# Performance work log

Measured on AMD Instinct MI355X. Metric: run time of the kernel, lower is better.

## Reference

```python
import jax, jax.numpy as jnp
import numpy as np

GRID_SIZE = 16
SPLINE_ORDER = 4
GRID_LO, GRID_HI = -1.0, 1.0
NUM_GRID = 2 * SPLINE_ORDER + GRID_SIZE + 1  # 25 knots
NUM_COEFFS = GRID_SIZE + SPLINE_ORDER        # 20 basis functions
B, IN_F, OUT_F = 2048, 512, 512


def _make_grid():
    h = (GRID_HI - GRID_LO) / GRID_SIZE
    t1 = -SPLINE_ORDER * h + GRID_LO
    t2 = (GRID_SIZE + SPLINE_ORDER + 1) * h + GRID_LO
    return jnp.linspace(t1, t2, NUM_GRID)


def _bspline_basis(x, grid):
    # x: [..., in]; returns [..., in, NUM_COEFFS] via De Boor recursion
    xe = x[..., None]
    bases = ((xe >= grid[:-1]) & (xe < grid[1:])).astype(x.dtype)
    for k in range(1, SPLINE_ORDER + 1):
        left = (xe - grid[:-k - 1]) / (grid[k:-1] - grid[:-k - 1]) * bases[..., :-1]
        right = (grid[k + 1:] - xe) / (grid[k + 1:] - grid[1:-k]) * bases[..., 1:]
        bases = left + right
    return bases


def setup_inputs() -> dict:
    key = jax.random.key(0)
    ks = jax.random.split(key, 5)
    fan = np.sqrt(1.0 / IN_F)
    return {
        "x": jax.random.normal(ks[0], (B, IN_F), jnp.float32),
        "prelu_weight": jax.random.normal(ks[1], (OUT_F, IN_F), jnp.float32) * 0.25,
        "base_weight": jax.random.uniform(ks[2], (OUT_F, IN_F), jnp.float32, -fan, fan),
        "spline_weight": jax.random.uniform(ks[3], (OUT_F, IN_F), jnp.float32, -fan, fan),
        "spline_coeffs": jax.random.normal(ks[4], (OUT_F, IN_F, NUM_COEFFS), jnp.float32) * 0.1,
    }


def reference(x, prelu_weight, base_weight, spline_weight, spline_coeffs):
    grid = _make_grid()
    xc = jnp.clip(x, GRID_LO, GRID_HI)
    pos = jax.nn.relu(xc)
    neg = xc - pos
    # base path: sum_j base_w[i,j]*(prelu_w[i,j]*neg[b,j] + pos[b,j])
    # fused: never materialize the [out, B, in] prelu output
    base = neg @ (base_weight * prelu_weight).T + pos @ base_weight.T  # [B, out]
    basis = _bspline_basis(xc, grid)  # [B, in, K]
    # spline path: fold spline_weight into coeffs, single contraction over (j,k)
    eff_coeffs = spline_weight[:, :, None] * spline_coeffs  # [out, in, K]
    spline = jnp.einsum('bjk,ijk->bi', basis, eff_coeffs)   # [B, out]
    return base + spline
```

## Files before the change

kernel.cpp:

```cpp
#include <hip/hip_runtime.h>


typedef _Float16 half_t;
typedef __attribute__((ext_vector_type(8))) _Float16 half8;
typedef __attribute__((ext_vector_type(4))) float floatx4;

#define B_DIM   2048
#define J_DIM   512
#define O_DIM   512
#define SLOTS   22
#define K_TOT   (J_DIM * SLOTS)
#define BM      256
#define BN      256
#define BK      32
#define KSPLIT  16

__device__ __forceinline__ void bspline5(float xc, int& k0, float Nv[5]) {
    const float invS = 7.68f;
    float u = (xc + 1.5f) * invS;
    int m = (int)u;
    m = min(max(m, 3), 19);
    k0 = m - 4;
    Nv[0] = 1.f; Nv[1] = 0.f; Nv[2] = 0.f; Nv[3] = 0.f; Nv[4] = 0.f;
#pragma unroll
    for (int d = 1; d <= 4; ++d) {
        float nw[5];
        float inv_d = 1.0f / (float)d;
#pragma unroll
        for (int r = 0; r < 5; ++r) {
            if (r > d) { nw[r] = 0.f; continue; }
            float kk = (float)(m - d + r);
            float acc = 0.f;
            if (r >= 1) acc += (u - kk) * Nv[r - 1];
            if (r < d)  acc += (kk + (float)(d + 1) - u) * Nv[r];
            nw[r] = acc * inv_d;
        }
#pragma unroll
        for (int r = 0; r < 5; ++r) Nv[r] = nw[r];
    }
}

__device__ __forceinline__ unsigned packh2(float a, float b) {
    half_t ha = (half_t)a, hb = (half_t)b;
    unsigned short ua = __builtin_bit_cast(unsigned short, ha);
    unsigned short ub = __builtin_bit_cast(unsigned short, hb);
    return (unsigned)ua | ((unsigned)ub << 16);
}

__global__ __launch_bounds__(256) void prep2(const float* __restrict__ x,
                                             const float* __restrict__ pw,
                                             const float* __restrict__ bw,
                                             const float* __restrict__ sw,
                                             const float* __restrict__ sc,
                                             half_t* __restrict__ A,
                                             half_t* __restrict__ Ct) {
    __shared__ half_t sbuf[2][128 * 88];
    int bid = blockIdx.x;
    int t = threadIdx.x;
    int sub = t >> 7;
    int jq  = t & 127;
    int j0  = jq * 4;

    if (bid < 256) {
        int i = bid * 2 + sub;
        size_t ij0 = (size_t)i * J_DIM + j0;
        float4 s4 = *(const float4*)(sw + ij0);
        float4 b4 = *(const float4*)(bw + ij0);
        float4 p4 = *(const float4*)(pw + ij0);
        const float4* sp4 = (const float4*)(sc + ij0 * 20);
        unsigned u[44];
#pragma unroll
        for (int jj = 0; jj < 4; ++jj) {
            float s = ((const float*)&s4)[jj];
            float b = ((const float*)&b4)[jj];
            float p = ((const float*)&p4)[jj];
#pragma unroll
            for (int v = 0; v < 5; ++v) {
                float4 c4 = sp4[jj * 5 + v];
                u[jj * 11 + v * 2 + 0] = packh2(s * c4.x, s * c4.y);
                u[jj * 11 + v * 2 + 1] = packh2(s * c4.z, s * c4.w);
            }
            u[jj * 11 + 10] = packh2(b * p, b);
        }
        uint4* dst = (uint4*)(Ct + (size_t)i * K_TOT + (size_t)j0 * SLOTS);
#pragma unroll
        for (int v = 0; v < 11; ++v)
            dst[v] = make_uint4(u[4 * v], u[4 * v + 1], u[4 * v + 2], u[4 * v + 3]);
        return;
    }

    int b0 = (bid - 256) * 2;
    int b = b0 + sub;
    float4 x4 = *(const float4*)(x + (size_t)b * J_DIM + j0);
    half_t* reg = &sbuf[sub][jq * 88];

    half8 z;
#pragma unroll
    for (int e = 0; e < 8; ++e) z[e] = (half_t)0.f;
#pragma unroll
    for (int v = 0; v < 11; ++v) *(half8*)(reg + v * 8) = z;

#pragma unroll
    for (int jj = 0; jj < 4; ++jj) {
        float xv = ((const float*)&x4)[jj];
        float xc = fminf(fmaxf(xv, -1.f), 1.f);
        float pos = fmaxf(xc, 0.f);
        float neg = xc - pos;
        int k0; float Nv[5];
        bspline5(xc, k0, Nv);
        half_t* rb = reg + jj * SLOTS;
#pragma unroll
        for (int rr = 0; rr < 5; ++rr) {
            int k = k0 + rr;
            if (k >= 0) rb[k] = (half_t)Nv[rr];
        }
        *(unsigned*)(rb + 20) = packh2(neg, pos);
    }
    __syncthreads();

    const uint4* src = (const uint4*)&sbuf[0][0];
    uint4* dst = (uint4*)(A + (size_t)b0 * K_TOT);
#pragma unroll
    for (int v = 0; v < 11; ++v) dst[v * 256 + t] = src[v * 256 + t];
}

__global__ __launch_bounds__(512, 2) void gemm256_f16(const half_t* __restrict__ A,
                                                      const half_t* __restrict__ Bt,
                                                      float* __restrict__ out) {
    constexpr int KS_LEN = K_TOT / KSPLIT;
    constexpr int KCH = KS_LEN / BK;

    __shared__ half_t As[3][BM * BK];
    __shared__ half_t Bs[3][BN * BK];

    int lid = blockIdx.x + 8 * (blockIdx.y + 2 * blockIdx.z);
    int c8 = lid & 7;
    int r2 = lid >> 3;
    int bz = c8 + 8 * (r2 & 1);
    int rr2 = r2 >> 1;
    int bx = rr2 & 7;
    int by = rr2 >> 3;

    int m0 = bx * BM;
    int n0 = by * BN;
    int ks = bz * KS_LEN;

    int t = threadIdx.x;
    int w = t >> 6;
    int l = t & 63;
    int wm = w >> 2, wn = w & 3;

    floatx4 acc[8][4] = {};

    int lrow = l >> 2;
    int lkof = (((l & 3) ^ ((l >> 3) & 3)) * 8);

    const half_t* gA = A + (size_t)m0 * K_TOT + ks;
    const half_t* gB = Bt + (size_t)n0 * K_TOT + ks;

    int q = l >> 4;
    int fr = l & 15;
    int qs = (q ^ ((fr >> 1) & 3)) * 8;

#define ISSUE_LOADS(c, p)                                                     \
    {                                                                         \
        int kb = (c) * BK;                                                    \
        _Pragma("unroll")                                                     \
        for (int s = 0; s < 2; ++s) {                                         \
            int r = (w * 2 + s) * 16 + lrow;                                  \
            __builtin_amdgcn_global_load_lds(                                 \
                (const __attribute__((address_space(1))) unsigned int*)       \
                    (gA + (size_t)r * K_TOT + kb + lkof),                     \
                (__attribute__((address_space(3))) unsigned int*)             \
                    (&As[p][0] + (w * 2 + s) * 512),                          \
                16, 0, 0);                                                    \
            __builtin_amdgcn_global_load_lds(                                 \
                (const __attribute__((address_space(1))) unsigned int*)       \
                    (gB + (size_t)r * K_TOT + kb + lkof),                     \
                (__attribute__((address_space(3))) unsigned int*)             \
                    (&Bs[p][0] + (w * 2 + s) * 512),                          \
                16, 0, 0);                                                    \
        }                                                                     \
    }

    ISSUE_LOADS(0, 0)
    ISSUE_LOADS(1, 1)

    int pb = 0;
    for (int c = 0; c < KCH; ++c) {
        if (c + 2 < KCH) {
            asm volatile("s_waitcnt vmcnt(4)" ::: "memory");
            __builtin_amdgcn_s_barrier();
            int pn = pb + 2; if (pn >= 3) pn -= 3;
            ISSUE_LOADS(c + 2, pn)
        } else if (c + 2 == KCH) {
            asm volatile("s_waitcnt vmcnt(4)" ::: "memory");
            __builtin_amdgcn_s_barrier();
        } else {
            asm volatile("s_waitcnt vmcnt(0)" ::: "memory");
            __builtin_amdgcn_s_barrier();
        }

        half8 af[8], bf[4];
#pragma unroll
        for (int nt = 0; nt < 4; ++nt)
            bf[nt] = *(const half8*)(&Bs[pb][0] + (wn * 64 + nt * 16 + fr) * BK + qs);
#pragma unroll
        for (int mt = 0; mt < 8; ++mt)
            af[mt] = *(const half8*)(&As[pb][0] + (wm * 128 + mt * 16 + fr) * BK + qs);

        __builtin_amdgcn_s_setprio(1);
#pragma unroll
        for (int mt = 0; mt < 8; ++mt)
#pragma unroll
            for (int nt = 0; nt < 4; ++nt)
                acc[mt][nt] = __builtin_amdgcn_mfma_f32_16x16x32_f16(
                    af[mt], bf[nt], acc[mt][nt], 0, 0, 0);
        __builtin_amdgcn_s_setprio(0);

        if (++pb == 3) pb = 0;
    }
#undef ISSUE_LOADS

    float* dst = out + (size_t)bz * ((size_t)B_DIM * O_DIM);
#pragma unroll
    for (int mt = 0; mt < 8; ++mt)
#pragma unroll
        for (int nt = 0; nt < 4; ++nt) {
            int rw = m0 + wm * 128 + mt * 16 + q * 4;
            int cc = n0 + wn * 64 + nt * 16 + fr;
#pragma unroll
            for (int rg = 0; rg < 4; ++rg)
                dst[(size_t)(rw + rg) * O_DIM + cc] = acc[mt][nt][rg];
        }
}

__global__ __launch_bounds__(256) void reduce16(const float* __restrict__ parts,
                                                float* __restrict__ out) {
    constexpr int N4 = B_DIM * O_DIM / 4;
    int i = blockIdx.x * 256 + threadIdx.x;
    const float4* p = (const float4*)parts;
    float4 a = p[i];
#pragma unroll
    for (int z = 1; z < KSPLIT; ++z) {
        float4 b = p[(size_t)z * N4 + i];
        a.x += b.x; a.y += b.y; a.z += b.z; a.w += b.w;
    }
    ((float4*)out)[i] = a;
}

__global__ __launch_bounds__(256) void kan_fallback(const float* __restrict__ x,
                                                    const float* __restrict__ pw,
                                                    const float* __restrict__ bw,
                                                    const float* __restrict__ sw,
                                                    const float* __restrict__ sc,
                                                    float* __restrict__ out) {
    __shared__ float s_neg[J_DIM], s_pos[J_DIM], s_bas[J_DIM][5];
    __shared__ int s_k0[J_DIM];
    int b = blockIdx.x;
    int t = threadIdx.x;
#pragma unroll
    for (int jj = 0; jj < 2; ++jj) {
        int j = t + jj * 256;
        float xv = x[(size_t)b * J_DIM + j];
        float xc = fminf(fmaxf(xv, -1.f), 1.f);
        float pos = fmaxf(xc, 0.f);
        s_pos[j] = pos;
        s_neg[j] = xc - pos;
        int k0; float Nv[5];
        bspline5(xc, k0, Nv);
        s_k0[j] = k0;
#pragma unroll
        for (int r = 0; r < 5; ++r) s_bas[j][r] = Nv[r];
    }
    __syncthreads();
    for (int i = t; i < O_DIM; i += 256) {
        float acc = 0.f;
        for (int j = 0; j < J_DIM; ++j) {
            size_t ij = (size_t)i * J_DIM + j;
            float bwv = bw[ij];
            acc += bwv * (pw[ij] * s_neg[j] + s_pos[j]);
            int k0 = s_k0[j];
            const float* cp = sc + ij * 20;
            float sp = 0.f;
#pragma unroll
            for (int r = 0; r < 5; ++r) {
                int k = k0 + r;
                if (k >= 0) sp += s_bas[j][r] * cp[k];
            }
            acc += sw[ij] * sp;
        }
        out[(size_t)b * O_DIM + i] = acc;
    }
}

extern "C" void kernel_launch(void* const* d_in, const int* in_sizes, int n_in,
                              void* d_out, int out_size, void* d_ws, size_t ws_size,
                              hipStream_t stream) {
    const float* x  = (const float*)d_in[0];
    const float* pw = (const float*)d_in[1];
    const float* bw = (const float*)d_in[2];
    const float* sw = (const float*)d_in[3];
    const float* sc = (const float*)d_in[4];
    float* out = (float*)d_out;

    const size_t abct = (size_t)(B_DIM + O_DIM) * K_TOT * sizeof(half_t);
    const size_t parts_bytes = (size_t)KSPLIT * B_DIM * O_DIM * sizeof(float);

    if (ws_size >= abct + parts_bytes) {
        half_t* A  = (half_t*)d_ws;
        half_t* Ct = A + (size_t)B_DIM * K_TOT;
        float* parts = (float*)((char*)d_ws + abct);

        prep2<<<256 + B_DIM / 2, 256, 0, stream>>>(x, pw, bw, sw, sc, A, Ct);
        dim3 g(B_DIM / BM, O_DIM / BN, KSPLIT);
        gemm256_f16<<<g, 512, 0, stream>>>(A, Ct, parts);
        reduce16<<<(B_DIM * O_DIM / 4) / 256, 256, 0, stream>>>(parts, out);
    } else {
        kan_fallback<<<B_DIM, 256, 0, stream>>>(x, pw, bw, sw, sc, out);
    }
}
```

Baseline: 140.1 us.

## Fuse B-spline basis generation into GEMM, padding per-feature slots to 32

```diff
diff --git a/kernel.cpp b/kernel.cpp
--- a/kernel.cpp
+++ b/kernel.cpp
@@ -8,12 +8,12 @@
 #define B_DIM   2048
 #define J_DIM   512
 #define O_DIM   512
-#define SLOTS   22
-#define K_TOT   (J_DIM * SLOTS)
+#define SLOT32  32
+#define KT32    (J_DIM * SLOT32)
 #define BM      256
 #define BN      256
-#define BK      32
 #define KSPLIT  16
+#define NPH     16
 
 __device__ __forceinline__ void bspline5(float xc, int& k0, float Nv[5]) {
     const float invS = 7.68f;
@@ -47,91 +47,51 @@
     return (unsigned)ua | ((unsigned)ub << 16);
 }
 
-__global__ __launch_bounds__(256) void prep2(const float* __restrict__ x,
-                                             const float* __restrict__ pw,
-                                             const float* __restrict__ bw,
-                                             const float* __restrict__ sw,
-                                             const float* __restrict__ sc,
-                                             half_t* __restrict__ A,
-                                             half_t* __restrict__ Ct) {
-    __shared__ half_t sbuf[2][128 * 88];
+__global__ __launch_bounds__(256) void prep_c32(const float* __restrict__ pw,
+                                                const float* __restrict__ bw,
+                                                const float* __restrict__ sw,
+                                                const float* __restrict__ sc,
+                                                half_t* __restrict__ Ct) {
     int bid = blockIdx.x;
     int t = threadIdx.x;
     int sub = t >> 7;
     int jq  = t & 127;
     int j0  = jq * 4;
 
-    if (bid < 256) {
-        int i = bid * 2 + sub;
-        size_t ij0 = (size_t)i * J_DIM + j0;
-        float4 s4 = *(const float4*)(sw + ij0);
-        float4 b4 = *(const float4*)(bw + ij0);
-        float4 p4 = *(const float4*)(pw + ij0);
-        const float4* sp4 = (const float4*)(sc + ij0 * 20);
-        unsigned u[44];
-#pragma unroll
-        for (int jj = 0; jj < 4; ++jj) {
-            float s = ((const float*)&s4)[jj];
-            float b = ((const float*)&b4)[jj];
-            float p = ((const float*)&p4)[jj];
-#pragma unroll
-            for (int v = 0; v < 5; ++v) {
-                float4 c4 = sp4[jj * 5 + v];
-                u[jj * 11 + v * 2 + 0] = packh2(s * c4.x, s * c4.y);
-                u[jj * 11 + v * 2 + 1] = packh2(s * c4.z, s * c4.w);
-            }
-            u[jj * 11 + 10] = packh2(b * p, b);
-        }
-        uint4* dst = (uint4*)(Ct + (size_t)i * K_TOT + (size_t)j0 * SLOTS);
-#pragma unroll
-        for (int v = 0; v < 11; ++v)
-            dst[v] = make_uint4(u[4 * v], u[4 * v + 1], u[4 * v + 2], u[4 * v + 3]);
-        return;
-    }
-
-    int b0 = (bid - 256) * 2;
-    int b = b0 + sub;
-    float4 x4 = *(const float4*)(x + (size_t)b * J_DIM + j0);
-    half_t* reg = &sbuf[sub][jq * 88];
-
-    half8 z;
-#pragma unroll
-    for (int e = 0; e < 8; ++e) z[e] = (half_t)0.f;
-#pragma unroll
-    for (int v = 0; v < 11; ++v) *(half8*)(reg + v * 8) = z;
-
+    int i = bid * 2 + sub;
+    size_t ij0 = (size_t)i * J_DIM + j0;
+    float4 s4 = *(const float4*)(sw + ij0);
+    float4 b4 = *(const float4*)(bw + ij0);
+    float4 p4 = *(const float4*)(pw + ij0);
+    const float4* sp4 = (const float4*)(sc + ij0 * 20);
+    unsigned u[64];
 #pragma unroll
     for (int jj = 0; jj < 4; ++jj) {
-        float xv = ((const float*)&x4)[jj];
-        float xc = fminf(fmaxf(xv, -1.f), 1.f);
-        float pos = fmaxf(xc, 0.f);
-        float neg = xc - pos;
-        int k0; float Nv[5];
-        bspline5(xc, k0, Nv);
-        half_t* rb = reg + jj * SLOTS;
-#pragma unroll
-        for (int rr = 0; rr < 5; ++rr) {
-            int k = k0 + rr;
-            if (k >= 0) rb[k] = (half_t)Nv[rr];
-        }
-        *(unsigned*)(rb + 20) = packh2(neg, pos);
-    }
-    __syncthreads();
-
-    const uint4* src = (const uint4*)&sbuf[0][0];
-    uint4* dst = (uint4*)(A + (size_t)b0 * K_TOT);
-#pragma unroll
-    for (int v = 0; v < 11; ++v) dst[v * 256 + t] = src[v * 256 + t];
-}
-
-__global__ __launch_bounds__(512, 2) void gemm256_f16(const half_t* __restrict__ A,
-                                                      const half_t* __restrict__ Bt,
-                                                      float* __restrict__ out) {
-    constexpr int KS_LEN = K_TOT / KSPLIT;
-    constexpr int KCH = KS_LEN / BK;
-
-    __shared__ half_t As[3][BM * BK];
-    __shared__ half_t Bs[3][BN * BK];
+        float s = ((const float*)&s4)[jj];
+        float b = ((const float*)&b4)[jj];
+        float p = ((const float*)&p4)[jj];
+#pragma unroll
+        for (int v = 0; v < 5; ++v) {
+            float4 c4 = sp4[jj * 5 + v];
+            u[jj * 16 + v * 2 + 0] = packh2(s * c4.x, s * c4.y);
+            u[jj * 16 + v * 2 + 1] = packh2(s * c4.z, s * c4.w);
+        }
+        u[jj * 16 + 10] = packh2(b * p, b);
+#pragma unroll
+        for (int v = 11; v < 16; ++v) u[jj * 16 + v] = 0u;
+    }
+    uint4* dst = (uint4*)(Ct + (size_t)i * KT32 + (size_t)j0 * SLOT32);
+#pragma unroll
+    for (int v = 0; v < 16; ++v)
+        dst[v] = make_uint4(u[4 * v], u[4 * v + 1], u[4 * v + 2], u[4 * v + 3]);
+}
+
+__global__ __launch_bounds__(512, 2) void kan_fused(const float* __restrict__ x,
+                                                    const half_t* __restrict__ Ct,
+                                                    float* __restrict__ out) {
+    __shared__ float  xt[32 * 256];
+    __shared__ half_t As[2][BM * 64];
+    __shared__ half_t Bs[2][BN * 64];
 
     int lid = blockIdx.x + 8 * (blockIdx.y + 2 * blockIdx.z);
     int c8 = lid & 7;
@@ -143,84 +103,104 @@
 
     int m0 = bx * BM;
     int n0 = by * BN;
-    int ks = bz * KS_LEN;
+    int j0 = bz * 32;
 
     int t = threadIdx.x;
-    int w = t >> 6;
-    int l = t & 63;
+    int w = t >> 6, l = t & 63;
     int wm = w >> 2, wn = w & 3;
+    int q = l >> 4, fr = l & 15;
+
+    const half_t* gB = Ct + (size_t)n0 * KT32 + (size_t)j0 * SLOT32;
+
+    int srow8 = l >> 3;
+    int lq    = (l & 7) ^ (srow8 & 7);
 
     floatx4 acc[8][4] = {};
 
-    int lrow = l >> 2;
-    int lkof = (((l & 3) ^ ((l >> 3) & 3)) * 8);
-
-    const half_t* gA = A + (size_t)m0 * K_TOT + ks;
-    const half_t* gB = Bt + (size_t)n0 * K_TOT + ks;
-
-    int q = l >> 4;
-    int fr = l & 15;
-    int qs = (q ^ ((fr >> 1) & 3)) * 8;
-
-#define ISSUE_LOADS(c, p)                                                     \
+#define ISSUE_BS(p, buf)                                                      \
     {                                                                         \
-        int kb = (c) * BK;                                                    \
         _Pragma("unroll")                                                     \
-        for (int s = 0; s < 2; ++s) {                                         \
-            int r = (w * 2 + s) * 16 + lrow;                                  \
+        for (int s = 0; s < 4; ++s) {                                         \
+            int rB = w * 32 + s * 8 + srow8;                                  \
             __builtin_amdgcn_global_load_lds(                                 \
                 (const __attribute__((address_space(1))) unsigned int*)       \
-                    (gA + (size_t)r * K_TOT + kb + lkof),                     \
+                    (gB + (size_t)rB * KT32 + (p) * 64 + lq * 8),             \
                 (__attribute__((address_space(3))) unsigned int*)             \
-                    (&As[p][0] + (w * 2 + s) * 512),                          \
-                16, 0, 0);                                                    \
-            __builtin_amdgcn_global_load_lds(                                 \
-                (const __attribute__((address_space(1))) unsigned int*)       \
-                    (gB + (size_t)r * K_TOT + kb + lkof),                     \
-                (__attribute__((address_space(3))) unsigned int*)             \
-                    (&Bs[p][0] + (w * 2 + s) * 512),                          \
+                    (&Bs[buf][(w * 32 + s * 8) * 64]),                        \
                 16, 0, 0);                                                    \
         }                                                                     \
     }
 
-    ISSUE_LOADS(0, 0)
-    ISSUE_LOADS(1, 1)
-
-    int pb = 0;
-    for (int c = 0; c < KCH; ++c) {
-        if (c + 2 < KCH) {
-            asm volatile("s_waitcnt vmcnt(4)" ::: "memory");
-            __builtin_amdgcn_s_barrier();
-            int pn = pb + 2; if (pn >= 3) pn -= 3;
-            ISSUE_LOADS(c + 2, pn)
-        } else if (c + 2 == KCH) {
-            asm volatile("s_waitcnt vmcnt(4)" ::: "memory");
-            __builtin_amdgcn_s_barrier();
-        } else {
-            asm volatile("s_waitcnt vmcnt(0)" ::: "memory");
-            __builtin_amdgcn_s_barrier();
-        }
-
-        half8 af[8], bf[4];
-#pragma unroll
-        for (int nt = 0; nt < 4; ++nt)
-            bf[nt] = *(const half8*)(&Bs[pb][0] + (wn * 64 + nt * 16 + fr) * BK + qs);
-#pragma unroll
-        for (int mt = 0; mt < 8; ++mt)
-            af[mt] = *(const half8*)(&As[pb][0] + (wm * 128 + mt * 16 + fr) * BK + qs);
-
-        __builtin_amdgcn_s_setprio(1);
-#pragma unroll
-        for (int mt = 0; mt < 8; ++mt)
+#define GEN_AS(p, buf)                                                        \
+    {                                                                         \
+        int bl = t & 255, jp = t >> 8;                                        \
+        int rx = bl & 7;                                                      \
+        float xv = xt[((p) * 2 + jp) * 256 + bl];                             \
+        float xc = fminf(fmaxf(xv, -1.f), 1.f);                               \
+        float pos = fmaxf(xc, 0.f);                                           \
+        float neg = xc - pos;                                                 \
+        int k0; float Nv[5];                                                  \
+        bspline5(xc, k0, Nv);                                                 \
+        half_t* rb = &As[buf][bl * 64];                                       \
+        half8 z8 = {};                                                        \
+        _Pragma("unroll")                                                     \
+        for (int kq = 0; kq < 4; ++kq)                                        \
+            *(half8*)(rb + ((jp * 4 + kq) ^ rx) * 8) = z8;                    \
+        *(unsigned*)(rb + ((jp * 4 + 2) ^ rx) * 8 + 4) = packh2(neg, pos);    \
+        _Pragma("unroll")                                                     \
+        for (int rr = 0; rr < 5; ++rr) {                                      \
+            int k = k0 + rr;                                                  \
+            if (k >= 0)                                                       \
+                rb[(((jp * 4 + (k >> 3)) ^ rx) * 8) + (k & 7)] =              \
+                    (half_t)Nv[rr];                                           \
+        }                                                                     \
+    }
+
+    ISSUE_BS(0, 0)
+#pragma unroll
+    for (int v = 0; v < 4; ++v) {
+        int r = v * 64 + (t >> 3);
+        int cq = t & 7;
+        float4 xv4 = *(const float4*)(x + (size_t)(m0 + r) * J_DIM + j0 + cq * 4);
+#pragma unroll
+        for (int c = 0; c < 4; ++c)
+            xt[(cq * 4 + c) * 256 + r] = ((const float*)&xv4)[c];
+    }
+    __syncthreads();
+    GEN_AS(0, 0)
+
+    for (int p = 0; p < NPH; ++p) {
+        asm volatile("s_waitcnt vmcnt(0) lgkmcnt(0)" ::: "memory");
+        __builtin_amdgcn_s_barrier();
+
+        if (p + 1 < NPH) ISSUE_BS(p + 1, (p + 1) & 1)
+
+        const half_t* Ab = &As[p & 1][0];
+        const half_t* Bb = &Bs[p & 1][0];
+#pragma unroll
+        for (int ks = 0; ks < 2; ++ks) {
+            half8 af[8], bf[4];
 #pragma unroll
             for (int nt = 0; nt < 4; ++nt)
-                acc[mt][nt] = __builtin_amdgcn_mfma_f32_16x16x32_f16(
-                    af[mt], bf[nt], acc[mt][nt], 0, 0, 0);
-        __builtin_amdgcn_s_setprio(0);
-
-        if (++pb == 3) pb = 0;
-    }
-#undef ISSUE_LOADS
+                bf[nt] = *(const half8*)(Bb + (wn * 64 + nt * 16 + fr) * 64
+                                            + (((ks * 4 + q) ^ (fr & 7)) * 8));
+#pragma unroll
+            for (int mt = 0; mt < 8; ++mt)
+                af[mt] = *(const half8*)(Ab + (wm * 128 + mt * 16 + fr) * 64
+                                            + (((ks * 4 + q) ^ (fr & 7)) * 8));
+            __builtin_amdgcn_s_setprio(1);
+#pragma unroll
+            for (int mt = 0; mt < 8; ++mt)
+#pragma unroll
+                for (int nt = 0; nt < 4; ++nt)
+                    acc[mt][nt] = __builtin_amdgcn_mfma_f32_16x16x32_f16(
+                        af[mt], bf[nt], acc[mt][nt], 0, 0, 0);
+            __builtin_amdgcn_s_setprio(0);
+        }
+        if (p + 1 < NPH) GEN_AS(p + 1, (p + 1) & 1)
+    }
+#undef GEN_AS
+#undef ISSUE_BS
 
     float* dst = out + (size_t)bz * ((size_t)B_DIM * O_DIM);
 #pragma unroll
@@ -304,17 +284,16 @@
     const float* sc = (const float*)d_in[4];
     float* out = (float*)d_out;
 
-    const size_t abct = (size_t)(B_DIM + O_DIM) * K_TOT * sizeof(half_t);
+    const size_t ct32_bytes  = (size_t)O_DIM * KT32 * sizeof(half_t);
     const size_t parts_bytes = (size_t)KSPLIT * B_DIM * O_DIM * sizeof(float);
 
-    if (ws_size >= abct + parts_bytes) {
-        half_t* A  = (half_t*)d_ws;
-        half_t* Ct = A + (size_t)B_DIM * K_TOT;
-        float* parts = (float*)((char*)d_ws + abct);
-
-        prep2<<<256 + B_DIM / 2, 256, 0, stream>>>(x, pw, bw, sw, sc, A, Ct);
+    if (ws_size >= ct32_bytes + parts_bytes) {
+        half_t* Ct32 = (half_t*)d_ws;
+        float* parts = (float*)((char*)d_ws + ct32_bytes);
+
+        prep_c32<<<O_DIM / 2, 256, 0, stream>>>(pw, bw, sw, sc, Ct32);
         dim3 g(B_DIM / BM, O_DIM / BN, KSPLIT);
-        gemm256_f16<<<g, 512, 0, stream>>>(A, Ct, parts);
+        kan_fused<<<g, 512, 0, stream>>>(x, Ct32, parts);
         reduce16<<<(B_DIM * O_DIM / 4) / 256, 256, 0, stream>>>(parts, out);
     } else {
         kan_fallback<<<B_DIM, 256, 0, stream>>>(x, pw, bw, sw, sc, out);
```

New measurement: 148.2 us. 5.7% more time.
